# Kernel tuning notes

Hardware: AMD Instinct MI355X
Metric: run time of the kernel (lower is better)

## Reference

```python
import jax, jax.numpy as jnp
import numpy as np

N = 100000
E = 1600000
NODE_IN = 8
EDGE_IN = 4
HID = 64
OUT = 4

# torch-initialized skip weights, in usage order (w2_1..w7_7)
SKIP_INIT = np.array([0.6, 0.4,
                      0.6, 0.4, 0.2,
                      0.6, 0.4, 0.2, 0.2,
                      0.6, 0.4, 0.2, 0.2, 0.2,
                      0.6, 0.4, 0.2, 0.2, 0.2, 0.2,
                      0.6, 0.4, 0.2, 0.2, 0.2, 0.2, 0.2], dtype=np.float32)

def _lin(key, fan_in, fan_out):
    b = 1.0 / np.sqrt(fan_in)
    k1, k2 = jax.random.split(key)
    W = jax.random.uniform(k1, (fan_in, fan_out), jnp.float32, -b, b)
    bias = jax.random.uniform(k2, (fan_out,), jnp.float32, -b, b)
    return W, bias

def setup_inputs() -> dict:
    key = jax.random.key(0)
    ks = jax.random.split(key, 20)
    x = jax.random.normal(ks[0], (N, NODE_IN), jnp.float32)
    edge_index = jax.random.randint(ks[1], (2, E), 0, N, jnp.int64)
    edge_attr = jax.random.normal(ks[2], (E, EDGE_IN), jnp.float32)
    # layer1
    Wm1, bm1 = _lin(ks[3], NODE_IN + EDGE_IN, HID)
    Wu1, bu1 = _lin(ks[4], NODE_IN + HID, HID)
    # mid layers (layers 2..6 of the torch module; layer7 is never used)
    Wm_mid, bm_mid, Wu_mid, bu_mid = [], [], [], []
    for i in range(5):
        Wm, bm = _lin(ks[5 + 2 * i], HID + EDGE_IN, HID)
        Wu, bu = _lin(ks[6 + 2 * i], HID + HID, HID)
        Wm_mid.append(Wm); bm_mid.append(bm); Wu_mid.append(Wu); bu_mid.append(bu)
    Wm_mid = jnp.stack(Wm_mid); bm_mid = jnp.stack(bm_mid)
    Wu_mid = jnp.stack(Wu_mid); bu_mid = jnp.stack(bu_mid)
    # last layer
    Wm_last, bm_last = _lin(ks[16], HID + EDGE_IN, OUT)
    Wu_last, bu_last = _lin(ks[17], HID + OUT, OUT)
    skip_weights = jnp.asarray(SKIP_INIT)
    return dict(x=x, edge_index=edge_index, edge_attr=edge_attr,
                Wm1=Wm1, bm1=bm1, Wu1=Wu1, bu1=bu1,
                Wm_mid=Wm_mid, bm_mid=bm_mid, Wu_mid=Wu_mid, bu_mid=bu_mid,
                Wm_last=Wm_last, bm_last=bm_last, Wu_last=Wu_last, bu_last=bu_last,
                skip_weights=skip_weights)

def _graph_layer(h, src, dst, edge_attr, Wm, bm, Wu, bu):
    # message: ReLU(Linear([h_src, e_attr]))  -> [E, out]
    m = jax.nn.relu(jnp.concatenate([h[src], edge_attr], axis=-1) @ Wm + bm)
    # sum-aggregate messages at destination nodes -> [N, out]
    agg = jax.ops.segment_sum(m, dst, num_segments=N)
    # node update: ReLU(Linear([h, agg]))
    return jax.nn.relu(jnp.concatenate([h, agg], axis=-1) @ Wu + bu)

def reference(x, edge_index, edge_attr,
              Wm1, bm1, Wu1, bu1,
              Wm_mid, bm_mid, Wu_mid, bu_mid,
              Wm_last, bm_last, Wu_last, bu_last,
              skip_weights):
    src, dst = edge_index[0], edge_index[1]
    sw = skip_weights
    L = lambda h, i: _graph_layer(h, src, dst, edge_attr,
                                  Wm_mid[i], bm_mid[i], Wu_mid[i], bu_mid[i])
    x1 = _graph_layer(x, src, dst, edge_attr, Wm1, bm1, Wu1, bu1)
    x2 = L(x1, 0)
    x2w = x1 * sw[0] + x2 * sw[1]
    x3 = L(x2w, 1)
    x3w = x1 * sw[2] + x2w * sw[3] + x3 * sw[4]
    x4 = L(x3w, 2)
    x4w = x1 * sw[5] + x2w * sw[6] + x3w * sw[7] + x4 * sw[8]
    x5 = L(x4w, 2)  # NOTE: source reuses layer4 here (faithful to bug)
    x5w = x1 * sw[9] + x2w * sw[10] + x3w * sw[11] + x4w * sw[12] + x5 * sw[13]
    x6 = L(x5w, 3)  # layer5
    x6w = x1 * sw[14] + x2w * sw[15] + x3w * sw[16] + x4w * sw[17] + x5w * sw[18] + x6 * sw[19]
    x7 = L(x6w, 4)  # layer6
    x7w = (x1 * sw[20] + x2w * sw[21] + x3w * sw[22] + x4w * sw[23]
           + x5w * sw[24] + x6w * sw[25] + x7 * sw[26])
    return _graph_layer(x7w, src, dst, edge_attr, Wm_last, bm_last, Wu_last, bu_last)
```

## Files before the change

### kernel.cpp

```cpp
#include <hip/hip_runtime.h>


#define WAVE 64

typedef __attribute__((ext_vector_type(4))) int int4v;

__device__ __forceinline__ unsigned short f2bf(float f) {
    unsigned b = __float_as_uint(f);
    unsigned r = b + 0x7FFFu + ((b >> 16) & 1u);
    return (unsigned short)(r >> 16);
}
__device__ __forceinline__ float bf2f(unsigned short u) {
    return __uint_as_float(((unsigned)u) << 16);
}
__device__ __forceinline__ int2 pack_ea(float4 a) {
    int2 r;
    r.x = (int)((unsigned)f2bf(a.x) | ((unsigned)f2bf(a.y) << 16));
    r.y = (int)((unsigned)f2bf(a.z) | ((unsigned)f2bf(a.w) << 16));
    return r;
}
__device__ __forceinline__ void store_nt16(int4* p, int s, int qx, int qy) {
    int4v v; v.x = s; v.y = qx; v.z = qy; v.w = 0;
    __builtin_nontemporal_store(v, reinterpret_cast<int4v*>(p));
}

__global__ __launch_bounds__(256) void hist_kernel(
    const int* __restrict__ ei, int* __restrict__ cnt, int E)
{
    int t = blockIdx.x * blockDim.x + threadIdx.x;
    int nt = gridDim.x * blockDim.x;
    for (int eb = t; eb < E; eb += 4 * nt) {
        int e1 = eb + nt, e2 = eb + 2 * nt, e3 = eb + 3 * nt;
        bool w1 = e1 < E, w2 = e2 < E, w3 = e3 < E;
        int d0 = ei[E + eb];
        int d1 = w1 ? ei[E + e1] : 0;
        int d2 = w2 ? ei[E + e2] : 0;
        int d3 = w3 ? ei[E + e3] : 0;
        atomicAdd(&cnt[d0], 1);
        if (w1) atomicAdd(&cnt[d1], 1);
        if (w2) atomicAdd(&cnt[d2], 1);
        if (w3) atomicAdd(&cnt[d3], 1);
    }
}

__global__ __launch_bounds__(256) void scan1_kernel(
    const int* __restrict__ cnt, int* __restrict__ out, int* __restrict__ bsum, int N)
{
    __shared__ int lds[256];
    int t = threadIdx.x;
    int base = blockIdx.x * 1024 + t * 4;
    int v0 = (base + 0 < N) ? cnt[base + 0] : 0;
    int v1 = (base + 1 < N) ? cnt[base + 1] : 0;
    int v2 = (base + 2 < N) ? cnt[base + 2] : 0;
    int v3 = (base + 3 < N) ? cnt[base + 3] : 0;
    int tsum = v0 + v1 + v2 + v3;
    lds[t] = tsum;
    __syncthreads();
    for (int off = 1; off < 256; off <<= 1) {
        int x = 0;
        if (t >= off) x = lds[t - off];
        __syncthreads();
        if (t >= off) lds[t] += x;
        __syncthreads();
    }
    int run = lds[t] - tsum;
    if (base + 0 < N) out[base + 0] = run; run += v0;
    if (base + 1 < N) out[base + 1] = run; run += v1;
    if (base + 2 < N) out[base + 2] = run; run += v2;
    if (base + 3 < N) out[base + 3] = run;
    if (t == 255) bsum[blockIdx.x] = lds[255];
}

__global__ __launch_bounds__(256) void scan2_kernel(int* __restrict__ bsum, int B)
{
    __shared__ int lds[256];
    __shared__ int carry;
    int t = threadIdx.x;
    if (t == 0) carry = 0;
    __syncthreads();
    for (int start = 0; start < B; start += 256) {
        int i = start + t;
        int v = (i < B) ? bsum[i] : 0;
        lds[t] = v;
        __syncthreads();
        for (int off = 1; off < 256; off <<= 1) {
            int x = 0;
            if (t >= off) x = lds[t - off];
            __syncthreads();
            if (t >= off) lds[t] += x;
            __syncthreads();
        }
        if (i < B) bsum[i] = carry + lds[t] - v;
        __syncthreads();
        if (t == 255) carry += lds[255];
        __syncthreads();
    }
}

__global__ __launch_bounds__(256) void scan3_kernel(
    int* __restrict__ rowptr, int* __restrict__ cursor,
    const int* __restrict__ bsum, int N, int E)
{
    int t = blockIdx.x * blockDim.x + threadIdx.x;
    int nt = gridDim.x * blockDim.x;
    for (int i = t; i < N; i += nt) {
        int v = rowptr[i] + bsum[i >> 10];
        rowptr[i] = v;
        cursor[i] = v;
    }
    if (t == 0) rowptr[N] = E;
}

__global__ __launch_bounds__(256) void scatter_kernel(
    const int* __restrict__ ei, const float* __restrict__ ea,
    int* __restrict__ cursor, int4* __restrict__ recs, int E)
{
    int t = blockIdx.x * blockDim.x + threadIdx.x;
    int nt = gridDim.x * blockDim.x;
    for (int eb = t; eb < E; eb += 4 * nt) {
        int e0 = eb, e1 = eb + nt, e2 = eb + 2 * nt, e3 = eb + 3 * nt;
        bool w1 = e1 < E, w2 = e2 < E, w3 = e3 < E;
        int d0 = ei[E + e0];
        int d1 = w1 ? ei[E + e1] : 0;
        int d2 = w2 ? ei[E + e2] : 0;
        int d3 = w3 ? ei[E + e3] : 0;
        int s0 = ei[e0];
        int s1 = w1 ? ei[e1] : 0;
        int s2 = w2 ? ei[e2] : 0;
        int s3 = w3 ? ei[e3] : 0;
        float4 a0 = *reinterpret_cast<const float4*>(ea + (size_t)4 * e0);
        float4 a1 = w1 ? *reinterpret_cast<const float4*>(ea + (size_t)4 * e1) : make_float4(0, 0, 0, 0);
        float4 a2 = w2 ? *reinterpret_cast<const float4*>(ea + (size_t)4 * e2) : make_float4(0, 0, 0, 0);
        float4 a3 = w3 ? *reinterpret_cast<const float4*>(ea + (size_t)4 * e3) : make_float4(0, 0, 0, 0);
        int p0 = atomicAdd(&cursor[d0], 1);
        int p1 = w1 ? atomicAdd(&cursor[d1], 1) : 0;
        int p2 = w2 ? atomicAdd(&cursor[d2], 1) : 0;
        int p3 = w3 ? atomicAdd(&cursor[d3], 1) : 0;
        int2 q0 = pack_ea(a0), q1 = pack_ea(a1), q2 = pack_ea(a2), q3 = pack_ea(a3);
        store_nt16(recs + p0, s0, q0.x, q0.y);
        if (w1) store_nt16(recs + p1, s1, q1.x, q1.y);
        if (w2) store_nt16(recs + p2, s2, q2.x, q2.y);
        if (w3) store_nt16(recs + p3, s3, q3.x, q3.y);
    }
}


template<int C>
__device__ __forceinline__ void stage_rows(
    const float* __restrict__ src, int rs, int base, int N, int t, float* As)
{
    constexpr int NFQ = C / 4;
    for (int idx = t; idx < 64 * NFQ; idx += 256) {
        int n = idx / NFQ, kq = idx % NFQ;
        int gn = min(base + n, N - 1);
        *reinterpret_cast<float4*>(As + n * 68 + 4 * kq) =
            *reinterpret_cast<const float4*>(src + (size_t)gn * rs + 4 * kq);
    }
}

template<int C>
__device__ __forceinline__ void stage_rows_bf(
    const unsigned short* __restrict__ src, int rs, int base, int N, int t, float* As)
{
    constexpr int NFQ = C / 4;
    for (int idx = t; idx < 64 * NFQ; idx += 256) {
        int n = idx / NFQ, kq = idx % NFQ;
        int gn = min(base + n, N - 1);
        ushort4 u = *reinterpret_cast<const ushort4*>(src + (size_t)gn * rs + 4 * kq);
        float4 v; v.x = bf2f(u.x); v.y = bf2f(u.y); v.z = bf2f(u.z); v.w = bf2f(u.w);
        *reinterpret_cast<float4*>(As + n * 68 + 4 * kq) = v;
    }
}

template<int C>
__device__ __forceinline__ void stage_w(
    const float* __restrict__ Wg, int t, float* Ws)
{
    const float4* wsrc = reinterpret_cast<const float4*>(Wg);
    float4* wdst = reinterpret_cast<float4*>(Ws);
    for (int idx = t; idx < C * 16; idx += 256) wdst[idx] = wsrc[idx];
}

template<int C>
__device__ __forceinline__ void compute_rm(
    const float* As, const float* Ws, int tx, int ty, float acc[4][4])
{
#pragma unroll 2
    for (int k = 0; k < C; k += 4) {
        float4 w0 = *reinterpret_cast<const float4*>(Ws + (k + 0) * 64 + 4 * tx);
        float4 w1 = *reinterpret_cast<const float4*>(Ws + (k + 1) * 64 + 4 * tx);
        float4 w2 = *reinterpret_cast<const float4*>(Ws + (k + 2) * 64 + 4 * tx);
        float4 w3 = *reinterpret_cast<const float4*>(Ws + (k + 3) * 64 + 4 * tx);
#pragma unroll
        for (int i = 0; i < 4; ++i) {
            float4 a = *reinterpret_cast<const float4*>(As + (4 * ty + i) * 68 + k);
            acc[i][0] = fmaf(a.x, w0.x, acc[i][0]);
            acc[i][1] = fmaf(a.x, w0.y, acc[i][1]);
            acc[i][2] = fmaf(a.x, w0.z, acc[i][2]);
            acc[i][3] = fmaf(a.x, w0.w, acc[i][3]);
            acc[i][0] = fmaf(a.y, w1.x, acc[i][0]);
            acc[i][1] = fmaf(a.y, w1.y, acc[i][1]);
            acc[i][2] = fmaf(a.y, w1.z, acc[i][2]);
            acc[i][3] = fmaf(a.y, w1.w, acc[i][3]);
            acc[i][0] = fmaf(a.z, w2.x, acc[i][0]);
            acc[i][1] = fmaf(a.z, w2.y, acc[i][1]);
            acc[i][2] = fmaf(a.z, w2.z, acc[i][2]);
            acc[i][3] = fmaf(a.z, w2.w, acc[i][3]);
            acc[i][0] = fmaf(a.w, w3.x, acc[i][0]);
            acc[i][1] = fmaf(a.w, w3.y, acc[i][1]);
            acc[i][2] = fmaf(a.w, w3.z, acc[i][2]);
            acc[i][3] = fmaf(a.w, w3.w, acc[i][3]);
        }
    }
}

template<int K1, bool ABF, bool HASB, bool RELU, bool SKIPP, bool UPDP, bool INITP, bool HASP, bool OUTBF>
__global__ __launch_bounds__(256) void lin4_kernel(
    const void* __restrict__ Av, const unsigned short* __restrict__ B,
    const float* __restrict__ W, const float* __restrict__ bias,
    float* __restrict__ out, unsigned short* __restrict__ Pb,
    const float* __restrict__ Wnext, const float* __restrict__ bnext,
    float* __restrict__ pout, int N,
    const float* __restrict__ sw, int csIdx, int ciIdx)
{
    __shared__ float As[64 * 68];
    __shared__ float Ws[64 * 64];
    int t = threadIdx.x;
    int tx = t & 15, ty = t >> 4;
    int base = blockIdx.x * 64;

    float acc[4][4];
    {
        float4 bv = *reinterpret_cast<const float4*>(bias + 4 * tx);
#pragma unroll
        for (int i = 0; i < 4; ++i) {
            acc[i][0] = bv.x; acc[i][1] = bv.y; acc[i][2] = bv.z; acc[i][3] = bv.w;
        }
    }

    if constexpr (ABF)
        stage_rows_bf<K1>((const unsigned short*)Av, K1, base, N, t, As);
    else
        stage_rows<K1>((const float*)Av, K1, base, N, t, As);
    stage_w<K1>(W, t, Ws);
    __syncthreads();
    compute_rm<K1>(As, Ws, tx, ty, acc);

    if constexpr (HASB) {
        __syncthreads();
        stage_rows_bf<64>(B, 64, base, N, t, As);
        stage_w<64>(W + (size_t)K1 * 64, t, Ws);
        __syncthreads();
        compute_rm<64>(As, Ws, tx, ty, acc);
    }

    float cs = 0.0f, ci = 0.0f;
    if (SKIPP) cs = sw[csIdx];
    if (UPDP || INITP) ci = sw[ciIdx];

    if constexpr (HASP) __syncthreads();

#pragma unroll
    for (int i = 0; i < 4; ++i) {
        int gn = base + 4 * ty + i;
        float r0 = acc[i][0], r1 = acc[i][1], r2 = acc[i][2], r3 = acc[i][3];
        if (RELU) {
            r0 = fmaxf(r0, 0.0f); r1 = fmaxf(r1, 0.0f);
            r2 = fmaxf(r2, 0.0f); r3 = fmaxf(r3, 0.0f);
        }
        size_t off = (size_t)gn * 64 + 4 * tx;
        float4 Pv = {0, 0, 0, 0};
        if (SKIPP && gn < N) {
            ushort4 pu = *reinterpret_cast<const ushort4*>(Pb + off);
            Pv.x = bf2f(pu.x); Pv.y = bf2f(pu.y); Pv.z = bf2f(pu.z); Pv.w = bf2f(pu.w);
            r0 = fmaf(cs, r0, Pv.x);
            r1 = fmaf(cs, r1, Pv.y);
            r2 = fmaf(cs, r2, Pv.z);
            r3 = fmaf(cs, r3, Pv.w);
        }
        if (gn < N) {
            if (OUTBF) {
                ushort4 u;
                u.x = f2bf(r0); u.y = f2bf(r1); u.z = f2bf(r2); u.w = f2bf(r3);
                *reinterpret_cast<ushort4*>(reinterpret_cast<unsigned short*>(out) + off) = u;
            } else {
                float4 r; r.x = r0; r.y = r1; r.z = r2; r.w = r3;
                *reinterpret_cast<float4*>(out + off) = r;
            }
            if (UPDP) {
                ushort4 pn;
                pn.x = f2bf(fmaf(ci, r0, Pv.x));
                pn.y = f2bf(fmaf(ci, r1, Pv.y));
                pn.z = f2bf(fmaf(ci, r2, Pv.z));
                pn.w = f2bf(fmaf(ci, r3, Pv.w));
                *reinterpret_cast<ushort4*>(Pb + off) = pn;
            }
            if (INITP) {
                ushort4 pn;
                pn.x = f2bf(ci * r0); pn.y = f2bf(ci * r1);
                pn.z = f2bf(ci * r2); pn.w = f2bf(ci * r3);
                *reinterpret_cast<ushort4*>(Pb + off) = pn;
            }
        }
        if (HASP) {
            float* as = As + (4 * ty + i) * 68 + 4 * tx;
            as[0] = r0; as[1] = r1; as[2] = r2; as[3] = r3;
        }
    }

    if constexpr (HASP) {
        stage_w<64>(Wnext, t, Ws);
        __syncthreads();
        float acc2[4][4];
        {
            float4 bv = *reinterpret_cast<const float4*>(bnext + 4 * tx);
#pragma unroll
            for (int i = 0; i < 4; ++i) {
                acc2[i][0] = bv.x; acc2[i][1] = bv.y; acc2[i][2] = bv.z; acc2[i][3] = bv.w;
            }
        }
        compute_rm<64>(As, Ws, tx, ty, acc2);
#pragma unroll
        for (int i = 0; i < 4; ++i) {
            int gn = base + 4 * ty + i;
            if (gn < N) {
                ushort4 u;
                u.x = f2bf(acc2[i][0]); u.y = f2bf(acc2[i][1]);
                u.z = f2bf(acc2[i][2]); u.w = f2bf(acc2[i][3]);
                *reinterpret_cast<ushort4*>(
                    reinterpret_cast<unsigned short*>(pout) + (size_t)gn * 64 + 4 * tx) = u;
            }
        }
    }
}

__global__ __launch_bounds__(256) void csr_agg_kernel(
    const int* __restrict__ rowptr, const int4* __restrict__ recs,
    const unsigned short* __restrict__ pb, const float* __restrict__ Wme,
    unsigned short* __restrict__ aggb, int N)
{
    int lane = threadIdx.x & 63;
    int g = lane >> 4;
    int q = lane & 15;
    int gwave = blockIdx.x * (blockDim.x >> 6) + (threadIdx.x >> 6);
    int nw = gridDim.x * (blockDim.x >> 6);
    float4 w0 = *reinterpret_cast<const float4*>(Wme + 0 * 64 + 4 * q);
    float4 w1 = *reinterpret_cast<const float4*>(Wme + 1 * 64 + 4 * q);
    float4 w2 = *reinterpret_cast<const float4*>(Wme + 2 * 64 + 4 * q);
    float4 w3 = *reinterpret_cast<const float4*>(Wme + 3 * 64 + 4 * q);

    for (int n = gwave; n < N; n += nw) {
        int beg = rowptr[n], end = rowptr[n + 1];
        int deg = end - beg;
        int nc = (deg + 3) >> 2;
        float4 acc = {0, 0, 0, 0};
        int4 rA = {0, 0, 0, 0}, rB = {0, 0, 0, 0};
        bool vA = (g < deg);
        bool vB = (4 + g < deg);
        if (vA) rA = recs[beg + g];
        if (vB) rB = recs[beg + 4 + g];
        ushort4 pA = *reinterpret_cast<const ushort4*>(pb + (size_t)rA.x * 64 + 4 * q);
        for (int c = 0; c < nc; ++c) {
            int4 rC = {0, 0, 0, 0};
            bool vC = (4 * (c + 2) + g) < deg;
            if (vC) rC = recs[beg + 4 * (c + 2) + g];
            ushort4 pB = *reinterpret_cast<const ushort4*>(pb + (size_t)rB.x * 64 + 4 * q);
            float ax = bf2f((unsigned short)(rA.y & 0xffff));
            float ay = bf2f((unsigned short)((unsigned)rA.y >> 16));
            float az = bf2f((unsigned short)(rA.z & 0xffff));
            float aw = bf2f((unsigned short)((unsigned)rA.z >> 16));
            float4 m;
            m.x = fmaf(ax, w0.x, fmaf(ay, w1.x, fmaf(az, w2.x, fmaf(aw, w3.x, bf2f(pA.x)))));
            m.y = fmaf(ax, w0.y, fmaf(ay, w1.y, fmaf(az, w2.y, fmaf(aw, w3.y, bf2f(pA.y)))));
            m.z = fmaf(ax, w0.z, fmaf(ay, w1.z, fmaf(az, w2.z, fmaf(aw, w3.z, bf2f(pA.z)))));
            m.w = fmaf(ax, w0.w, fmaf(ay, w1.w, fmaf(az, w2.w, fmaf(aw, w3.w, bf2f(pA.w)))));
            float f = vA ? 1.0f : 0.0f;
            acc.x = fmaf(f, fmaxf(m.x, 0.0f), acc.x);
            acc.y = fmaf(f, fmaxf(m.y, 0.0f), acc.y);
            acc.z = fmaf(f, fmaxf(m.z, 0.0f), acc.z);
            acc.w = fmaf(f, fmaxf(m.w, 0.0f), acc.w);
            vA = vB; rA = rB; pA = pB;
            vB = vC; rB = rC;
        }
        acc.x += __shfl_xor(acc.x, 16); acc.y += __shfl_xor(acc.y, 16);
        acc.z += __shfl_xor(acc.z, 16); acc.w += __shfl_xor(acc.w, 16);
        acc.x += __shfl_xor(acc.x, 32); acc.y += __shfl_xor(acc.y, 32);
        acc.z += __shfl_xor(acc.z, 32); acc.w += __shfl_xor(acc.w, 32);
        if (g == 0) {
            ushort4 u;
            u.x = f2bf(acc.x); u.y = f2bf(acc.y); u.z = f2bf(acc.z); u.w = f2bf(acc.w);
            *reinterpret_cast<ushort4*>(aggb + (size_t)n * 64 + 4 * q) = u;
        }
    }
}

__global__ __launch_bounds__(256) void edge_kernel(
    const int* __restrict__ ei, const float* __restrict__ ea,
    const unsigned short* __restrict__ pb, const float* __restrict__ Wme,
    float* __restrict__ agg, int E)
{
    int lane = threadIdx.x & 63;
    int gwave = blockIdx.x * (blockDim.x >> 6) + (threadIdx.x >> 6);
    int nw = gridDim.x * (blockDim.x >> 6);
    float w0 = Wme[0 * 64 + lane];
    float w1 = Wme[1 * 64 + lane];
    float w2 = Wme[2 * 64 + lane];
    float w3 = Wme[3 * 64 + lane];
    for (int e = gwave; e < E; e += nw) {
        int s = ei[e];
        int d = ei[E + e];
        float4 a = *reinterpret_cast<const float4*>(ea + (size_t)4 * e);
        float v = bf2f(pb[(size_t)s * 64 + lane]);
        v = fmaf(a.x, w0, v);
        v = fmaf(a.y, w1, v);
        v = fmaf(a.z, w2, v);
        v = fmaf(a.w, w3, v);
        v = fmaxf(v, 0.0f);
        atomicAdd(agg + (size_t)d * 64 + lane, v);
    }
}

__global__ __launch_bounds__(256) void f2bf_kernel(
    const float* __restrict__ in, unsigned short* __restrict__ out, int n)
{
    int t = blockIdx.x * blockDim.x + threadIdx.x;
    int nt = gridDim.x * blockDim.x;
    for (int i = t; i < n; i += nt) out[i] = f2bf(in[i]);
}

__global__ __launch_bounds__(256) void pl_kernel(
    const unsigned short* __restrict__ A, const float* __restrict__ W,
    const float* __restrict__ bias, float* __restrict__ out, int N)
{
    __shared__ float Wl[64 * 4];
    __shared__ float bl[4];
    for (int i = threadIdx.x; i < 256; i += blockDim.x) Wl[i] = W[i];
    if (threadIdx.x < 4) bl[threadIdx.x] = bias[threadIdx.x];
    __syncthreads();
    int t = blockIdx.x * blockDim.x + threadIdx.x;
    int nt = gridDim.x * blockDim.x;
    for (int idx = t; idx < N * 4; idx += nt) {
        int n = idx >> 2, f = idx & 3;
        float acc = bl[f];
        const unsigned short* ar = A + (size_t)n * 64;
#pragma unroll 4
        for (int kk = 0; kk < 16; ++kk) {
            ushort4 u = *reinterpret_cast<const ushort4*>(ar + 4 * kk);
            acc = fmaf(bf2f(u.x), Wl[(4 * kk + 0) * 4 + f], acc);
            acc = fmaf(bf2f(u.y), Wl[(4 * kk + 1) * 4 + f], acc);
            acc = fmaf(bf2f(u.z), Wl[(4 * kk + 2) * 4 + f], acc);
            acc = fmaf(bf2f(u.w), Wl[(4 * kk + 3) * 4 + f], acc);
        }
        out[idx] = acc;
    }
}

__global__ __launch_bounds__(256) void csr_agg4_kernel(
    const int* __restrict__ rowptr, const int4* __restrict__ recs,
    const float* __restrict__ p4, const float* __restrict__ Wme,
    float* __restrict__ agg4, int N)
{
    float w[16];
#pragma unroll
    for (int i = 0; i < 16; ++i) w[i] = Wme[i];
    int t = blockIdx.x * blockDim.x + threadIdx.x;
    int nt = gridDim.x * blockDim.x;
    for (int n = t; n < N; n += nt) {
        int beg = rowptr[n], end = rowptr[n + 1];
        float4 acc = {0, 0, 0, 0};
        for (int j = beg; j < end; ++j) {
            int4 r = recs[j];
            float ax = bf2f((unsigned short)(r.y & 0xffff));
            float ay = bf2f((unsigned short)((unsigned)r.y >> 16));
            float az = bf2f((unsigned short)(r.z & 0xffff));
            float aw = bf2f((unsigned short)((unsigned)r.z >> 16));
            float4 pv = *reinterpret_cast<const float4*>(p4 + (size_t)4 * r.x);
            float vx = pv.x + ax * w[0] + ay * w[4] + az * w[8]  + aw * w[12];
            float vy = pv.y + ax * w[1] + ay * w[5] + az * w[9]  + aw * w[13];
            float vz = pv.z + ax * w[2] + ay * w[6] + az * w[10] + aw * w[14];
            float vw = pv.w + ax * w[3] + ay * w[7] + az * w[11] + aw * w[15];
            acc.x += fmaxf(vx, 0.0f);
            acc.y += fmaxf(vy, 0.0f);
            acc.z += fmaxf(vz, 0.0f);
            acc.w += fmaxf(vw, 0.0f);
        }
        *reinterpret_cast<float4*>(agg4 + (size_t)4 * n) = acc;
    }
}

__global__ __launch_bounds__(256) void edge4_kernel(
    const int* __restrict__ ei, const float* __restrict__ ea,
    const float* __restrict__ p4, const float* __restrict__ Wme,
    float* __restrict__ agg4, int E)
{
    int lane = threadIdx.x & 63;
    int f = lane & 3;
    int gwave = blockIdx.x * (blockDim.x >> 6) + (threadIdx.x >> 6);
    int nw = gridDim.x * (blockDim.x >> 6);
    float w0 = Wme[0 * 4 + f];
    float w1 = Wme[1 * 4 + f];
    float w2 = Wme[2 * 4 + f];
    float w3 = Wme[3 * 4 + f];
    for (int e0 = gwave * 16; e0 < E; e0 += nw * 16) {
        int e = e0 + (lane >> 2);
        if (e < E) {
            int s = ei[e];
            int d = ei[E + e];
            float4 a = *reinterpret_cast<const float4*>(ea + (size_t)4 * e);
            float v = p4[(size_t)s * 4 + f];
            v = fmaf(a.x, w0, v);
            v = fmaf(a.y, w1, v);
            v = fmaf(a.z, w2, v);
            v = fmaf(a.w, w3, v);
            v = fmaxf(v, 0.0f);
            atomicAdd(agg4 + (size_t)d * 4 + f, v);
        }
    }
}

__global__ __launch_bounds__(256) void ul_kernel(
    const unsigned short* __restrict__ A, const float* __restrict__ agg4,
    const float* __restrict__ W , const float* __restrict__ bias,
    float* __restrict__ out, int N)
{
    __shared__ float Wl[68 * 4];
    __shared__ float bl[4];
    for (int i = threadIdx.x; i < 68 * 4; i += blockDim.x) Wl[i] = W[i];
    if (threadIdx.x < 4) bl[threadIdx.x] = bias[threadIdx.x];
    __syncthreads();
    int t = blockIdx.x * blockDim.x + threadIdx.x;
    int nt = gridDim.x * blockDim.x;
    for (int idx = t; idx < N * 4; idx += nt) {
        int n = idx >> 2, f = idx & 3;
        float acc = bl[f];
        const unsigned short* ar = A + (size_t)n * 64;
#pragma unroll 4
        for (int kk = 0; kk < 16; ++kk) {
            ushort4 u = *reinterpret_cast<const ushort4*>(ar + 4 * kk);
            acc = fmaf(bf2f(u.x), Wl[(4 * kk + 0) * 4 + f], acc);
            acc = fmaf(bf2f(u.y), Wl[(4 * kk + 1) * 4 + f], acc);
            acc = fmaf(bf2f(u.z), Wl[(4 * kk + 2) * 4 + f], acc);
            acc = fmaf(bf2f(u.w), Wl[(4 * kk + 3) * 4 + f], acc);
        }
        float4 g = *reinterpret_cast<const float4*>(agg4 + (size_t)n * 4);
        acc = fmaf(g.x, Wl[(64 + 0) * 4 + f], acc);
        acc = fmaf(g.y, Wl[(64 + 1) * 4 + f], acc);
        acc = fmaf(g.z, Wl[(64 + 2) * 4 + f], acc);
        acc = fmaf(g.w, Wl[(64 + 3) * 4 + f], acc);
        out[idx] = fmaxf(acc, 0.0f);
    }
}

extern "C" void kernel_launch(void* const* d_in, const int* in_sizes, int n_in,
                              void* d_out, int out_size, void* d_ws, size_t ws_size,
                              hipStream_t stream)
{
    const float* x      = (const float*)d_in[0];
    const int*   ei     = (const int*)d_in[1];
    const float* ea     = (const float*)d_in[2];
    const float* Wm1    = (const float*)d_in[3];
    const float* bm1    = (const float*)d_in[4];
    const float* Wu1    = (const float*)d_in[5];
    const float* bu1    = (const float*)d_in[6];
    const float* Wm_mid = (const float*)d_in[7];
    const float* bm_mid = (const float*)d_in[8];
    const float* Wu_mid = (const float*)d_in[9];
    const float* bu_mid = (const float*)d_in[10];
    const float* WmL    = (const float*)d_in[11];
    const float* bmL    = (const float*)d_in[12];
    const float* WuL    = (const float*)d_in[13];
    const float* buL    = (const float*)d_in[14];
    const float* sw     = (const float*)d_in[15];

    const int N = in_sizes[0] / 8;
    const int E = in_sizes[2] / 4;

    float* ws = (float*)d_ws;
    size_t nh = (size_t)N * 64;
    float* p    = ws;
    float* agg  = ws + nh;
    float* xwA  = ws + 2 * nh;
    float* xwB  = ws + 3 * nh;
    unsigned short* Pb = (unsigned short*)(ws + 4 * nh);
    float* p4   = agg;
    float* agg4 = agg + (size_t)N * 4;

    int4*  recs  = (int4*)(ws + 5 * nh);
    int*   rowptr= (int*)(recs + E);
    int*   cursor= rowptr + N + 1;
    int*   bsum  = cursor + N;
    size_t need_bytes = 5 * nh * 4 + (size_t)E * 16 + ((size_t)2 * N + 1 + 1024) * 4;
    bool use_csr = ws_size >= need_bytes;

    dim3 blk(256);
    dim3 gEdge(2048), g4(1024);
    dim3 gLin((N + 63) / 64);
    const float* nul = nullptr;

    if (use_csr) {
        int B = (N + 1023) / 1024;
        hipMemsetAsync(cursor, 0, (size_t)N * 4, stream);
        hist_kernel<<<gEdge, blk, 0, stream>>>(ei, cursor, E);
        scan1_kernel<<<dim3(B), blk, 0, stream>>>(cursor, rowptr, bsum, N);
        scan2_kernel<<<dim3(1), blk, 0, stream>>>(bsum, B);
        scan3_kernel<<<dim3(256), blk, 0, stream>>>(rowptr, cursor, bsum, N, E);
        scatter_kernel<<<gEdge, blk, 0, stream>>>(ei, ea, cursor, recs, E);
    }

    auto edge_pass = [&](const float* pp, const float* Wme, float* aggout) {
        if (use_csr) {
            csr_agg_kernel<<<gEdge, blk, 0, stream>>>(
                rowptr, recs, (const unsigned short*)pp, Wme,
                (unsigned short*)aggout, N);
        } else {
            float* aggf = (float*)recs;
            hipMemsetAsync(aggf, 0, nh * sizeof(float), stream);
            edge_kernel<<<gEdge, blk, 0, stream>>>(
                ei, ea, (const unsigned short*)pp, Wme, aggf, E);
            f2bf_kernel<<<dim3(2048), blk, 0, stream>>>(
                aggf, (unsigned short*)aggout, (int)nh);
        }
    };

    struct MidStep { int mi; const float* in; float* out; int cs; int ci; };
    MidStep steps[6] = {
        {0, xwA, xwB, 1,  3},
        {1, xwB, xwA, 4,  7},
        {2, xwA, xwB, 8,  12},
        {2, xwB, xwA, 13, 18},
        {3, xwA, xwB, 19, 25},
        {4, xwB, xwA, 26, 0},
    };

    lin4_kernel<8, false, false, false, false, false, false, false, true><<<gLin, blk, 0, stream>>>(
        x, nullptr, Wm1, bm1, p, nullptr, nul, nul, nullptr, N, sw, 0, 0);
    edge_pass(p, Wm1 + 8 * 64, agg);
    lin4_kernel<8, false, true, true, false, false, true, true, true><<<gLin, blk, 0, stream>>>(
        x, (const unsigned short*)agg, Wu1, bu1, xwA, Pb,
        Wm_mid + (size_t)0 * 68 * 64, bm_mid + (size_t)0 * 64, p, N, sw, 0, 0);

    for (int li = 0; li < 6; ++li) {
        const MidStep& st = steps[li];
        const float* Wm = Wm_mid + (size_t)st.mi * 68 * 64;
        const float* Wu = Wu_mid + (size_t)st.mi * 128 * 64;
        const float* bu = bu_mid + (size_t)st.mi * 64;
        edge_pass(p, Wm + 64 * 64, agg);
        if (li < 5) {
            int nmi = steps[li + 1].mi;
            lin4_kernel<64, true, true, true, true, true, false, true, true><<<gLin, blk, 0, stream>>>(
                st.in, (const unsigned short*)agg, Wu, bu, st.out, Pb,
                Wm_mid + (size_t)nmi * 68 * 64, bm_mid + (size_t)nmi * 64, p, N,
                sw, st.cs, st.ci);
        } else {
            lin4_kernel<64, true, true, true, true, false, false, false, true><<<gLin, blk, 0, stream>>>(
                st.in, (const unsigned short*)agg, Wu, bu, st.out, Pb,
                nul, nul, nullptr, N, sw, st.cs, 0);
        }
    }
    float* x7w = steps[5].out;

    pl_kernel<<<g4, blk, 0, stream>>>((const unsigned short*)x7w, WmL, bmL, p4, N);
    if (use_csr) {
        csr_agg4_kernel<<<g4, blk, 0, stream>>>(rowptr, recs, p4, WmL + 64 * 4, agg4, N);
    } else {
        hipMemsetAsync(agg4, 0, (size_t)N * 4 * sizeof(float), stream);
        edge4_kernel<<<gEdge, blk, 0, stream>>>(ei, ea, p4, WmL + 64 * 4, agg4, E);
    }
    ul_kernel<<<g4, blk, 0, stream>>>((const unsigned short*)x7w, agg4, WuL, buL, (float*)d_out, N);
}
```

Before: 857.6 us.

## Split CSR scatter into two-pass bucketed radix-style scatter for locality

Replaces the single random scatter of edge records into CSR order with a two-pass scheme. Edges are first bucketed by destination block of 128 nodes into a temporary buffer, using coarse bucket counters from an extended histogram and a single-block scan. A second pass then scatters each bucketed chunk to its final CSR position, so writes stay within a small region. This targets the scattered 16-byte stores and the contended per-node atomics, at the cost of an extra E-sized temporary buffer, an extra read/write pass and two more kernel launches.

```diff
diff --git a/kernel.cpp b/kernel.cpp
--- a/kernel.cpp
+++ b/kernel.cpp
@@ -2,8 +2,7 @@
 
 
 #define WAVE 64
-
-typedef __attribute__((ext_vector_type(4))) int int4v;
+#define BSH 7
 
 __device__ __forceinline__ unsigned short f2bf(float f) {
     unsigned b = __float_as_uint(f);
@@ -19,13 +18,9 @@
     r.y = (int)((unsigned)f2bf(a.z) | ((unsigned)f2bf(a.w) << 16));
     return r;
 }
-__device__ __forceinline__ void store_nt16(int4* p, int s, int qx, int qy) {
-    int4v v; v.x = s; v.y = qx; v.z = qy; v.w = 0;
-    __builtin_nontemporal_store(v, reinterpret_cast<int4v*>(p));
-}
-
-__global__ __launch_bounds__(256) void hist_kernel(
-    const int* __restrict__ ei, int* __restrict__ cnt, int E)
+
+__global__ __launch_bounds__(256) void hist2_kernel(
+    const int* __restrict__ ei, int* __restrict__ cnt, int* __restrict__ bcnt, int E)
 {
     int t = blockIdx.x * blockDim.x + threadIdx.x;
     int nt = gridDim.x * blockDim.x;
@@ -37,9 +32,10 @@
         int d2 = w2 ? ei[E + e2] : 0;
         int d3 = w3 ? ei[E + e3] : 0;
         atomicAdd(&cnt[d0], 1);
-        if (w1) atomicAdd(&cnt[d1], 1);
-        if (w2) atomicAdd(&cnt[d2], 1);
-        if (w3) atomicAdd(&cnt[d3], 1);
+        atomicAdd(&bcnt[d0 >> BSH], 1);
+        if (w1) { atomicAdd(&cnt[d1], 1); atomicAdd(&bcnt[d1 >> BSH], 1); }
+        if (w2) { atomicAdd(&cnt[d2], 1); atomicAdd(&bcnt[d2 >> BSH], 1); }
+        if (w3) { atomicAdd(&cnt[d3], 1); atomicAdd(&bcnt[d3 >> BSH], 1); }
     }
 }
 
@@ -111,9 +107,36 @@
     if (t == 0) rowptr[N] = E;
 }
 
-__global__ __launch_bounds__(256) void scatter_kernel(
+__global__ __launch_bounds__(256) void bscan_kernel(
+    const int* __restrict__ bcnt, int* __restrict__ bcur, int NB)
+{
+    __shared__ int lds[256];
+    __shared__ int carry;
+    int t = threadIdx.x;
+    if (t == 0) carry = 0;
+    __syncthreads();
+    for (int start = 0; start < NB; start += 256) {
+        int i = start + t;
+        int v = (i < NB) ? bcnt[i] : 0;
+        lds[t] = v;
+        __syncthreads();
+        for (int off = 1; off < 256; off <<= 1) {
+            int x = 0;
+            if (t >= off) x = lds[t - off];
+            __syncthreads();
+            if (t >= off) lds[t] += x;
+            __syncthreads();
+        }
+        if (i < NB) bcur[i] = carry + lds[t] - v;
+        __syncthreads();
+        if (t == 255) carry += lds[255];
+        __syncthreads();
+    }
+}
+
+__global__ __launch_bounds__(256) void scatterA_kernel(
     const int* __restrict__ ei, const float* __restrict__ ea,
-    int* __restrict__ cursor, int4* __restrict__ recs, int E)
+    int* __restrict__ bcur, int4* __restrict__ tmp, int E)
 {
     int t = blockIdx.x * blockDim.x + threadIdx.x;
     int nt = gridDim.x * blockDim.x;
@@ -132,15 +155,30 @@
         float4 a1 = w1 ? *reinterpret_cast<const float4*>(ea + (size_t)4 * e1) : make_float4(0, 0, 0, 0);
         float4 a2 = w2 ? *reinterpret_cast<const float4*>(ea + (size_t)4 * e2) : make_float4(0, 0, 0, 0);
         float4 a3 = w3 ? *reinterpret_cast<const float4*>(ea + (size_t)4 * e3) : make_float4(0, 0, 0, 0);
-        int p0 = atomicAdd(&cursor[d0], 1);
-        int p1 = w1 ? atomicAdd(&cursor[d1], 1) : 0;
-        int p2 = w2 ? atomicAdd(&cursor[d2], 1) : 0;
-        int p3 = w3 ? atomicAdd(&cursor[d3], 1) : 0;
+        int p0 = atomicAdd(&bcur[d0 >> BSH], 1);
+        int p1 = w1 ? atomicAdd(&bcur[d1 >> BSH], 1) : 0;
+        int p2 = w2 ? atomicAdd(&bcur[d2 >> BSH], 1) : 0;
+        int p3 = w3 ? atomicAdd(&bcur[d3 >> BSH], 1) : 0;
         int2 q0 = pack_ea(a0), q1 = pack_ea(a1), q2 = pack_ea(a2), q3 = pack_ea(a3);
-        store_nt16(recs + p0, s0, q0.x, q0.y);
-        if (w1) store_nt16(recs + p1, s1, q1.x, q1.y);
-        if (w2) store_nt16(recs + p2, s2, q2.x, q2.y);
-        if (w3) store_nt16(recs + p3, s3, q3.x, q3.y);
+        tmp[p0] = make_int4(s0, q0.x, q0.y, d0);
+        if (w1) tmp[p1] = make_int4(s1, q1.x, q1.y, d1);
+        if (w2) tmp[p2] = make_int4(s2, q2.x, q2.y, d2);
+        if (w3) tmp[p3] = make_int4(s3, q3.x, q3.y, d3);
+    }
+}
+
+__global__ __launch_bounds__(256) void scatterB_kernel(
+    const int4* __restrict__ tmp, int* __restrict__ cursor,
+    int4* __restrict__ recs, int E)
+{
+    for (int c = blockIdx.x; c * 2048 < E; c += gridDim.x) {
+        int beg = c * 2048;
+        int end = min(beg + 2048, E);
+        for (int j = beg + (int)threadIdx.x; j < end; j += blockDim.x) {
+            int4 r = tmp[j];
+            int pos = atomicAdd(&cursor[r.w], 1);
+            recs[pos] = make_int4(r.x, r.y, r.z, 0);
+        }
     }
 }
 
@@ -574,6 +612,7 @@
 
     const int N = in_sizes[0] / 8;
     const int E = in_sizes[2] / 4;
+    const int NB = (N + (1 << BSH) - 1) >> BSH;
 
     float* ws = (float*)d_ws;
     size_t nh = (size_t)N * 64;
@@ -586,10 +625,14 @@
     float* agg4 = agg + (size_t)N * 4;
 
     int4*  recs  = (int4*)(ws + 5 * nh);
-    int*   rowptr= (int*)(recs + E);
+    int4*  tmp   = recs + E;
+    int*   rowptr= (int*)(tmp + E);
     int*   cursor= rowptr + N + 1;
     int*   bsum  = cursor + N;
-    size_t need_bytes = 5 * nh * 4 + (size_t)E * 16 + ((size_t)2 * N + 1 + 1024) * 4;
+    int*   bcnt  = bsum + 1024;
+    int*   bcur  = bcnt + NB;
+    size_t need_bytes = 5 * nh * 4 + (size_t)E * 32
+                      + ((size_t)2 * N + 1 + 1024 + 2 * (size_t)NB) * 4;
     bool use_csr = ws_size >= need_bytes;
 
     dim3 blk(256);
@@ -599,12 +642,14 @@
 
     if (use_csr) {
         int B = (N + 1023) / 1024;
-        hipMemsetAsync(cursor, 0, (size_t)N * 4, stream);
-        hist_kernel<<<gEdge, blk, 0, stream>>>(ei, cursor, E);
+        hipMemsetAsync(cursor, 0, ((size_t)N + 1024 + NB) * 4, stream);
+        hist2_kernel<<<gEdge, blk, 0, stream>>>(ei, cursor, bcnt, E);
         scan1_kernel<<<dim3(B), blk, 0, stream>>>(cursor, rowptr, bsum, N);
         scan2_kernel<<<dim3(1), blk, 0, stream>>>(bsum, B);
         scan3_kernel<<<dim3(256), blk, 0, stream>>>(rowptr, cursor, bsum, N, E);
-        scatter_kernel<<<gEdge, blk, 0, stream>>>(ei, ea, cursor, recs, E);
+        bscan_kernel<<<dim3(1), blk, 0, stream>>>(bcnt, bcur, NB);
+        scatterA_kernel<<<gEdge, blk, 0, stream>>>(ei, ea, bcur, tmp, E);
+        scatterB_kernel<<<dim3(1024), blk, 0, stream>>>(tmp, cursor, recs, E);
     }
 
     auto edge_pass = [&](const float* pp, const float* Wme, float* aggout) {
```

After: 1.547 ms. +80.4%, slower.
